# Kernel tuning notes

Measured on AMD Instinct MI355X. Metric: run time of the kernel, lower is better.

The kernel has to match this reference:

```python
import jax, jax.numpy as jnp
import numpy as np

B, S, D, H = 2, 1024, 1024, 8
HD = D // H            # head_dim = 128
NBUCKETS = 64          # bucket_size (number of hash buckets)
NEG = -1e30


def setup_inputs() -> dict:
    key = jax.random.key(0)
    ks = jax.random.split(key, 10)
    scale = D ** -0.5
    return {
        "x": jax.random.normal(ks[0], (B, S, D), dtype=jnp.float32),
        "Wq": jax.random.normal(ks[1], (D, D), dtype=jnp.float32) * scale,
        "bq": jnp.zeros((D,), dtype=jnp.float32),
        "Wk": jax.random.normal(ks[2], (D, D), dtype=jnp.float32) * scale,
        "bk": jnp.zeros((D,), dtype=jnp.float32),
        "Wv": jax.random.normal(ks[3], (D, D), dtype=jnp.float32) * scale,
        "bv": jnp.zeros((D,), dtype=jnp.float32),
        "Wo": jax.random.normal(ks[4], (D, D), dtype=jnp.float32) * scale,
        "bo": jnp.zeros((D,), dtype=jnp.float32),
        "hash_proj": jax.random.normal(ks[5], (H, HD, NBUCKETS), dtype=jnp.float32),
    }


def reference(x, Wq, bq, Wk, bk, Wv, bv, Wo, bo, hash_proj):
    b, s, d = x.shape
    n = b * s  # buckets gather (batch, token) pairs jointly -> flatten batch into tokens

    def split_heads(y):  # [B,S,D] -> [H, B*S, HD]
        return y.reshape(b, s, H, HD).transpose(2, 0, 1, 3).reshape(H, n, HD)

    q = split_heads(x @ Wq + bq)
    k = split_heads(x @ Wk + bk)
    v = split_heads(x @ Wv + bv)

    # learned LSH routing: argmax over hash projections per head
    hash_scores = jnp.einsum('hnd,hdf->hnf', q, hash_proj)
    buckets = jnp.argmax(hash_scores, axis=-1)  # [H, N] int

    # per-bucket attention == masked dense attention with same-bucket mask
    dots = jnp.einsum('hnd,hmd->hnm', q, k) / (HD ** 0.5)  # [H,N,N]
    same = buckets[:, :, None] == buckets[:, None, :]
    attn = jax.nn.softmax(jnp.where(same, dots, NEG), axis=-1)
    o = jnp.einsum('hnm,hmd->hnd', attn, v)  # [H,N,HD]

    out = o.reshape(H, b, s, HD).transpose(1, 2, 0, 3).reshape(b, s, d)
    return out @ Wo + bo
```

## Files before the change

### kernel.cpp

```cpp
#include <hip/hip_runtime.h>
#include <stdint.h>

typedef __attribute__((ext_vector_type(8))) short short8;
typedef __attribute__((ext_vector_type(4))) short short4v;
typedef __attribute__((ext_vector_type(4))) float float4v;
typedef unsigned short u16;

#define N_TOK 2048
#define D_MODEL 1024
#define N_HEAD 8
#define HDIM 128
#define N_BUCKET 64
#define WL_CAP 2048
#define ATTN_BLOCKS 384

__device__ __forceinline__ u16 f2bf(float f) {
  uint32_t u = __float_as_uint(f);
  uint32_t r = u + 0x7fffu + ((u >> 16) & 1u);
  return (u16)(r >> 16);
}
__device__ __forceinline__ float bf2f(u16 h) {
  return __uint_as_float(((uint32_t)h) << 16);
}

__device__ __forceinline__ void async_load16(const void* g, void* l) {
  __builtin_amdgcn_global_load_lds(
      (const __attribute__((address_space(1))) void*)g,
      (__attribute__((address_space(3))) void*)l, 16, 0, 0);
}

__device__ __forceinline__ int xcd_swz(int bid, int nwg) {
  return (bid & 7) * (nwg >> 3) + (bid >> 3);
}

__global__ __launch_bounds__(256) void split_cast_kernel(
    const float* __restrict__ in, u16* __restrict__ hi, u16* __restrict__ lo,
    int n) {
  int i = blockIdx.x * 256 + threadIdx.x;
  if (i >= n) return;
  float v = in[i];
  u16 h = f2bf(v);
  hi[i] = h;
  if (lo) lo[i] = f2bf(v - bf2f(h));
}

__global__ __launch_bounds__(256) void transpose_all_kernel(
    const float* __restrict__ Wq, const float* __restrict__ Wk,
    const float* __restrict__ Wv, const float* __restrict__ Wo,
    u16* __restrict__ wqt_hi, u16* __restrict__ wqt_lo,
    u16* __restrict__ kvt, u16* __restrict__ wot) {
  __shared__ float tile[32][33];
  const int z = blockIdx.z;
  const float* in = (z == 0) ? Wq : (z == 1) ? Wk : (z == 2) ? Wv : Wo;
  u16* hi = (z == 0) ? wqt_hi
            : (z == 1) ? kvt
            : (z == 2) ? (kvt + (size_t)1024 * 1024) : wot;
  u16* lo = (z == 0) ? wqt_lo : nullptr;
  const int C = 1024, R = 1024;
  int c0 = blockIdx.x * 32, r0 = blockIdx.y * 32;
  int tx = threadIdx.x & 31, ty = threadIdx.x >> 5;
#pragma unroll
  for (int i = 0; i < 4; i++) {
    int rl = ty + i * 8;
    tile[rl][tx] = in[(size_t)(r0 + rl) * C + c0 + tx];
  }
  __syncthreads();
#pragma unroll
  for (int i = 0; i < 4; i++) {
    int cl = ty + i * 8;
    float v = tile[tx][cl];
    size_t oidx = (size_t)(c0 + cl) * R + r0 + tx;
    u16 h = f2bf(v);
    hi[oidx] = h;
    if (lo) lo[oidx] = f2bf(v - bf2f(h));
  }
}

template <int BM>
__device__ __forceinline__ void stage_tiles2(const u16* A, const u16* Bt,
                                             u16* As, u16* Bs, int bm, int bn,
                                             int K, int ko, int wave, int lane) {
  const int arow = lane >> 2;
  const int acolb = (lane & 3) * 16;
  constexpr int ACH = BM / 16;
  constexpr int PC = (ACH + 8) / 4;
#pragma unroll
  for (int cc = 0; cc < PC; cc++) {
    int idx = wave * PC + cc;
    if (idx < ACH) {
      int row = idx * 16 + arow;
      const char* g = (const char*)A + ((size_t)(bm + row) * K + ko) * 2 + acolb;
      async_load16(g, (char*)As + idx * 1024);
    } else {
      int row = (idx - ACH) * 16 + arow;
      const char* g = (const char*)Bt + ((size_t)(bn + row) * K + ko) * 2 + acolb;
      async_load16(g, (char*)Bs + (idx - ACH) * 1024);
    }
  }
}

template <int BM>
__global__ __launch_bounds__(256) void gemm_bf16_kernel(
    const u16* __restrict__ A, const u16* __restrict__ Bt,
    float* __restrict__ C, const float* __restrict__ bias,
    const float* __restrict__ bias2, u16* __restrict__ kbf,
    u16* __restrict__ vbf, int N, int K, int flags) {
  constexpr int MI = BM / 32;
  __shared__ __align__(16) u16 As[2][BM * 32];
  __shared__ __align__(16) u16 Bs[2][128 * 32];
  const int tid = threadIdx.x;
  const int wave = tid >> 6, lane = tid & 63;
  const int lhi = lane >> 4, llo = lane & 15;
  const int nbn = N >> 7;
  const int bid = xcd_swz(blockIdx.x, gridDim.x);
  const int bm = (bid / nbn) * BM;
  const int bn = (bid % nbn) << 7;
  const int wm = (BM == 128) ? (wave >> 1) * 64 : (wave & 1) * 32;
  const int wn = (BM == 128) ? (wave & 1) * 64 : (wave >> 1) * 64;

  float4v acc[MI][4];
#pragma unroll
  for (int mi = 0; mi < MI; mi++)
#pragma unroll
    for (int ni = 0; ni < 4; ni++)
#pragma unroll
      for (int r = 0; r < 4; r++) acc[mi][ni][r] = 0.f;

  stage_tiles2<BM>(A, Bt, As[0], Bs[0], bm, bn, K, 0, wave, lane);
  __syncthreads();
  const int nk = K >> 5;
  for (int t = 0; t < nk; t++) {
    const int cur = t & 1;
    if (t + 1 < nk)
      stage_tiles2<BM>(A, Bt, As[cur ^ 1], Bs[cur ^ 1], bm, bn, K,
                       (t + 1) << 5, wave, lane);
    short8 af[MI], bfr[4];
#pragma unroll
    for (int i = 0; i < MI; i++)
      af[i] = *(const short8*)&As[cur][(wm + i * 16 + llo) * 32 + lhi * 8];
#pragma unroll
    for (int i = 0; i < 4; i++)
      bfr[i] = *(const short8*)&Bs[cur][(wn + i * 16 + llo) * 32 + lhi * 8];
#pragma unroll
    for (int mi = 0; mi < MI; mi++)
#pragma unroll
      for (int ni = 0; ni < 4; ni++)
        acc[mi][ni] = __builtin_amdgcn_mfma_f32_16x16x32_bf16(af[mi], bfr[ni],
                                                              acc[mi][ni], 0, 0, 0);
    __syncthreads();
  }

#pragma unroll
  for (int mi = 0; mi < MI; mi++)
#pragma unroll
    for (int ni = 0; ni < 4; ni++) {
      int row0 = bm + wm + mi * 16 + lhi * 4;
      int col = bn + wn + ni * 16 + llo;
      if (flags & 8) {
        u16* dst = (col < 1024) ? kbf : vbf;
        int c = col & 1023;
        float bb = (col < 1024) ? bias[c] : bias2[c];
#pragma unroll
        for (int r = 0; r < 4; r++)
          dst[(size_t)(row0 + r) * 1024 + c] = f2bf(acc[mi][ni][r] + bb);
      } else {
        float bb = (flags & 2) ? bias[col] : 0.f;
        float* cp = C + (size_t)row0 * N + col;
#pragma unroll
        for (int r = 0; r < 4; r++) cp[(size_t)r * N] = acc[mi][ni][r] + bb;
      }
    }
}

__global__ __launch_bounds__(256) void gemm3_bf16_kernel(
    const u16* __restrict__ A0, const u16* __restrict__ A1,
    const u16* __restrict__ B0, const u16* __restrict__ B1,
    float* __restrict__ C, const float* __restrict__ bias,
    u16* __restrict__ bf_out, int N, int K) {
  constexpr int MI = 2;
  __shared__ __align__(16) u16 S3[2][12288];
  const int tid = threadIdx.x;
  const int wave = tid >> 6, lane = tid & 63;
  const int lhi = lane >> 4, llo = lane & 15;
  const int nbn = N >> 7;
  const int bid = xcd_swz(blockIdx.x, gridDim.x);
  const int bm = (bid / nbn) * 64;
  const int bn = (bid % nbn) << 7;
  const int wm = (wave & 1) * 32;
  const int wn = (wave >> 1) * 64;
  const int arow = lane >> 2;
  const int acolb = (lane & 3) * 16;

  float4v acc[MI][4];
#pragma unroll
  for (int mi = 0; mi < MI; mi++)
#pragma unroll
    for (int ni = 0; ni < 4; ni++)
#pragma unroll
      for (int r = 0; r < 4; r++) acc[mi][ni][r] = 0.f;

  auto stage = [&](int b, int ko) {
    char* base = (char*)&S3[b][0];
#pragma unroll
    for (int cc = 0; cc < 6; cc++) {
      int idx = wave * 6 + cc;
      const u16* src;
      int row;
      char* dst;
      if (idx < 4) {
        src = A0; row = bm + idx * 16 + arow; dst = base + idx * 1024;
      } else if (idx < 8) {
        src = A1; row = bm + (idx - 4) * 16 + arow; dst = base + 4096 + (idx - 4) * 1024;
      } else if (idx < 16) {
        src = B0; row = bn + (idx - 8) * 16 + arow; dst = base + 8192 + (idx - 8) * 1024;
      } else {
        src = B1; row = bn + (idx - 16) * 16 + arow; dst = base + 16384 + (idx - 16) * 1024;
      }
      async_load16((const char*)src + ((size_t)row * K + ko) * 2 + acolb, dst);
    }
  };

  stage(0, 0);
  __syncthreads();
  const int nk = K >> 5;
  for (int t = 0; t < nk; t++) {
    const int cur = t & 1;
    if (t + 1 < nk) stage(cur ^ 1, (t + 1) << 5);
    const u16* Sc = &S3[cur][0];
    short8 afh[MI], afl[MI], bfh[4], bfl[4];
#pragma unroll
    for (int i = 0; i < MI; i++) {
      afh[i] = *(const short8*)&Sc[(wm + i * 16 + llo) * 32 + lhi * 8];
      afl[i] = *(const short8*)&Sc[2048 + (wm + i * 16 + llo) * 32 + lhi * 8];
    }
#pragma unroll
    for (int i = 0; i < 4; i++) {
      bfh[i] = *(const short8*)&Sc[4096 + (wn + i * 16 + llo) * 32 + lhi * 8];
      bfl[i] = *(const short8*)&Sc[8192 + (wn + i * 16 + llo) * 32 + lhi * 8];
    }
#pragma unroll
    for (int mi = 0; mi < MI; mi++)
#pragma unroll
      for (int ni = 0; ni < 4; ni++)
        acc[mi][ni] = __builtin_amdgcn_mfma_f32_16x16x32_bf16(afh[mi], bfh[ni],
                                                              acc[mi][ni], 0, 0, 0);
#pragma unroll
    for (int mi = 0; mi < MI; mi++)
#pragma unroll
      for (int ni = 0; ni < 4; ni++)
        acc[mi][ni] = __builtin_amdgcn_mfma_f32_16x16x32_bf16(afh[mi], bfl[ni],
                                                              acc[mi][ni], 0, 0, 0);
#pragma unroll
    for (int mi = 0; mi < MI; mi++)
#pragma unroll
      for (int ni = 0; ni < 4; ni++)
        acc[mi][ni] = __builtin_amdgcn_mfma_f32_16x16x32_bf16(afl[mi], bfh[ni],
                                                              acc[mi][ni], 0, 0, 0);
    __syncthreads();
  }

#pragma unroll
  for (int mi = 0; mi < MI; mi++)
#pragma unroll
    for (int ni = 0; ni < 4; ni++) {
      int row0 = bm + wm + mi * 16 + lhi * 4;
      int col = bn + wn + ni * 16 + llo;
      float bb = bias[col];
#pragma unroll
      for (int r = 0; r < 4; r++) {
        float v = acc[mi][ni][r] + bb;
        C[(size_t)(row0 + r) * N + col] = v;
        bf_out[(size_t)(row0 + r) * N + col] = f2bf(v);
      }
    }
}

__global__ __launch_bounds__(256) void hash_argmax_kernel(
    const float* __restrict__ Qf, const float* __restrict__ proj,
    int* __restrict__ bucket) {
  __shared__ float sQ[64 * 128];
  __shared__ float sP[128 * 64];
  const int tid = threadIdx.x;
  const int h = blockIdx.y;
  const int n0 = blockIdx.x * 64;
#pragma unroll
  for (int p = 0; p < 8; p++) {
    int e = p * 1024 + tid * 4;
    int tok = e >> 7, d0 = e & 127;
    float4v v = *(const float4v*)&Qf[(size_t)(n0 + tok) * D_MODEL + h * HDIM + d0];
    int blk = (d0 >> 2) ^ ((tok >> 2) & 7);
    *(float4v*)&sQ[tok * 128 + blk * 4] = v;
  }
#pragma unroll
  for (int p = 0; p < 8; p++) {
    int e = p * 1024 + tid * 4;
    float4v v = *(const float4v*)&proj[(size_t)h * (HDIM * N_BUCKET) + e];
    *(float4v*)&sP[e] = v;
  }
  __syncthreads();

  const int tgrp = tid & 15, fgrp = tid >> 4;
  const int t0 = tgrp * 4, f0 = fgrp * 4;
  float accs[4][4];
#pragma unroll
  for (int i = 0; i < 4; i++)
#pragma unroll
    for (int f = 0; f < 4; f++) accs[i][f] = 0.f;

  for (int d0 = 0; d0 < 128; d0 += 4) {
    int blk = (d0 >> 2) ^ (tgrp & 7);
    float4v qv[4], pv[4];
#pragma unroll
    for (int i = 0; i < 4; i++)
      qv[i] = *(const float4v*)&sQ[(t0 + i) * 128 + blk * 4];
#pragma unroll
    for (int j = 0; j < 4; j++)
      pv[j] = *(const float4v*)&sP[(d0 + j) * 64 + f0];
#pragma unroll
    for (int i = 0; i < 4; i++)
#pragma unroll
      for (int f = 0; f < 4; f++)
        accs[i][f] += qv[i][0] * pv[0][f] + qv[i][1] * pv[1][f] +
                      qv[i][2] * pv[2][f] + qv[i][3] * pv[3][f];
  }

  __syncthreads();
  float* vals = sQ;
  int* idxs = (int*)(sQ + 64 * 17);
#pragma unroll
  for (int i = 0; i < 4; i++) {
    float bv = accs[i][0];
    int bi = f0;
#pragma unroll
    for (int f = 1; f < 4; f++)
      if (accs[i][f] > bv) { bv = accs[i][f]; bi = f0 + f; }
    vals[(t0 + i) * 17 + fgrp] = bv;
    idxs[(t0 + i) * 17 + fgrp] = bi;
  }
  __syncthreads();
  if (tid < 64) {
    float bv = vals[tid * 17];
    int bi = idxs[tid * 17];
#pragma unroll
    for (int g = 1; g < 16; g++) {
      float v = vals[tid * 17 + g];
      int id = idxs[tid * 17 + g];
      if (v > bv || (v == bv && id < bi)) { bv = v; bi = id; }
    }
    bucket[h * N_TOK + n0 + tid] = bi;
  }
}

__global__ __launch_bounds__(64) void bucket_count_kernel(
    const int* __restrict__ bucket, int* __restrict__ counts) {
  int hb = blockIdx.x;
  int h = hb >> 6, b = hb & 63;
  int lane = threadIdx.x;
  int cnt = 0;
  for (int t = 0; t < N_TOK; t += 64) {
    bool match = bucket[h * N_TOK + t + lane] == b;
    unsigned long long mask = __ballot(match);
    cnt += __popcll(mask);
  }
  if (lane == 0) counts[hb] = cnt;
}

__global__ __launch_bounds__(512) void build_wl_kernel(
    const int* __restrict__ counts, int* __restrict__ offsets,
    int* __restrict__ wl, int* __restrict__ wl_count) {
  __shared__ int sc[512];
  int tid = threadIdx.x;
  int cnt = counts[tid];
  sc[tid] = cnt;
  __syncthreads();
  for (int o = 1; o < 512; o <<= 1) {
    int v = (tid >= o) ? sc[tid - o] : 0;
    __syncthreads();
    sc[tid] += v;
    __syncthreads();
  }
  offsets[tid] = sc[tid] - cnt;
  __syncthreads();
  int nq = (cnt + 15) >> 4;
  sc[tid] = nq;
  __syncthreads();
  for (int o = 1; o < 512; o <<= 1) {
    int v = (tid >= o) ? sc[tid - o] : 0;
    __syncthreads();
    sc[tid] += v;
    __syncthreads();
  }
  int base = sc[tid] - nq;
  int h = tid >> 6, b = tid & 63;
  for (int i = 0; i < nq; i++) wl[base + i] = (h << 13) | (b << 7) | i;
  if (tid == 511) wl_count[0] = sc[511];
}

__global__ __launch_bounds__(64) void bucket_fill_kernel(
    const int* __restrict__ bucket, const int* __restrict__ offsets,
    int* __restrict__ perm) {
  int hb = blockIdx.x;
  int h = hb >> 6, b = hb & 63;
  int lane = threadIdx.x;
  int base = offsets[hb];
  for (int t = 0; t < N_TOK; t += 64) {
    int tok = t + lane;
    bool match = bucket[h * N_TOK + tok] == b;
    unsigned long long mask = __ballot(match);
    if (match) {
      int pos = base + __popcll(mask & ((1ull << lane) - 1ull));
      perm[pos] = tok;
    }
    base += __popcll(mask);
  }
}

__global__ __launch_bounds__(256) void gather_vt_kernel(
    const u16* __restrict__ vbb, const int* __restrict__ perm,
    u16* __restrict__ Vts) {
  __shared__ u16 lds[64][72];
  int bid = blockIdx.x;
  int h = bid >> 6;
  int ptile = (bid & 63) >> 1;
  int d0 = (bid & 1) * 64;
  int pos0 = ptile * 64;
  int t = threadIdx.x;
#pragma unroll
  for (int i = 0; i < 2; i++) {
    int unit = t + 256 * i;
    int p = unit >> 3, seg = unit & 7;
    int tok = perm[h * N_TOK + pos0 + p];
    short8 v = *(const short8*)&vbb[(size_t)tok * D_MODEL + h * HDIM + d0 + seg * 8];
    *(short8*)&lds[p][seg * 8] = v;
  }
  __syncthreads();
#pragma unroll
  for (int i = 0; i < 8; i++) {
    int unit = t + 256 * i;
    int drow = unit >> 5, pp = unit & 31;
    uint32_t val = (uint32_t)lds[2 * pp][drow] |
                   ((uint32_t)lds[2 * pp + 1][drow] << 16);
    uint32_t* dst = (uint32_t*)&Vts[(size_t)(h * HDIM + d0 + drow) * N_TOK + pos0];
    dst[pp] = val;
  }
}

__global__ __launch_bounds__(256) void attn_bucket_kernel(
    const u16* __restrict__ qbb, const u16* __restrict__ kbb,
    const u16* __restrict__ Vts, const int* __restrict__ perm,
    const int* __restrict__ offsets, const int* __restrict__ counts,
    const int* __restrict__ wl, const int* __restrict__ wl_count,
    u16* __restrict__ ob) {
  const int wave = threadIdx.x >> 6, lane = threadIdx.x & 63;
  const int lhi = lane >> 4, llo = lane & 15;
  const int wslot = blockIdx.x * 4 + wave;
  const int NW = ATTN_BLOCKS * 4;
  const int cnt = wl_count[0];
  __shared__ __align__(16) u16 P_lds[4][16][64];
  const float scale = 0.08838834764831845f;

  for (int e = wslot; e < cnt; e += NW) {
    int ent = wl[e];
    int h = ent >> 13, qt = ent & 127;
    int hb = (h << 6) | ((ent >> 7) & 63);
    int off = offsets[hb];
    int bs = counts[hb];
    int offh = off - h * N_TOK;
    int qbase = qt * 16;

    int qr = qbase + llo;
    int tokq = perm[off + min(qr, bs - 1)];
    const u16* qrow = &qbb[(size_t)tokq * D_MODEL + h * HDIM];
    short8 qf[4];
#pragma unroll
    for (int kf = 0; kf < 4; kf++)
      qf[kf] = *(const short8*)&qrow[kf * 32 + lhi * 8];

    float m[4], l[4];
#pragma unroll
    for (int r = 0; r < 4; r++) { m[r] = -INFINITY; l[r] = 0.f; }
    float4v accO[8];
#pragma unroll
    for (int d = 0; d < 8; d++)
#pragma unroll
      for (int r = 0; r < 4; r++) accO[d][r] = 0.f;

    for (int c0 = 0; c0 < bs; c0 += 64) {
      float4v sc[4];
#pragma unroll
      for (int nf = 0; nf < 4; nf++)
#pragma unroll
        for (int r = 0; r < 4; r++) sc[nf][r] = 0.f;
#pragma unroll
      for (int nf = 0; nf < 4; nf++) {
        int kcol = c0 + nf * 16 + llo;
        int tokk = perm[off + min(kcol, bs - 1)];
        const u16* krow = &kbb[(size_t)tokk * D_MODEL + h * HDIM];
#pragma unroll
        for (int kf = 0; kf < 4; kf++) {
          short8 kfr = *(const short8*)&krow[kf * 32 + lhi * 8];
          sc[nf] = __builtin_amdgcn_mfma_f32_16x16x32_bf16(qf[kf], kfr, sc[nf], 0, 0, 0);
        }
      }

      float tmax[4];
#pragma unroll
      for (int r = 0; r < 4; r++) tmax[r] = -INFINITY;
#pragma unroll
      for (int nf = 0; nf < 4; nf++) {
        bool valid = (c0 + nf * 16 + llo) < bs;
#pragma unroll
        for (int r = 0; r < 4; r++) {
          float v = valid ? sc[nf][r] * scale : -1e30f;
          sc[nf][r] = v;
          tmax[r] = fmaxf(tmax[r], v);
        }
      }
#pragma unroll
      for (int r = 0; r < 4; r++)
#pragma unroll
        for (int o = 1; o < 16; o <<= 1)
          tmax[r] = fmaxf(tmax[r], __shfl_xor(tmax[r], o));

      float resc[4], psum[4];
#pragma unroll
      for (int r = 0; r < 4; r++) {
        float mn = fmaxf(m[r], tmax[r]);
        resc[r] = __expf(m[r] - mn);
        m[r] = mn;
        psum[r] = 0.f;
      }
#pragma unroll
      for (int nf = 0; nf < 4; nf++)
#pragma unroll
        for (int r = 0; r < 4; r++) {
          float p = __expf(sc[nf][r] - m[r]);
          psum[r] += p;
          P_lds[wave][lhi * 4 + r][nf * 16 + llo] = f2bf(p);
        }
#pragma unroll
      for (int r = 0; r < 4; r++) {
#pragma unroll
        for (int o = 1; o < 16; o <<= 1) psum[r] += __shfl_xor(psum[r], o);
        l[r] = l[r] * resc[r] + psum[r];
      }
#pragma unroll
      for (int d = 0; d < 8; d++)
#pragma unroll
        for (int r = 0; r < 4; r++) accO[d][r] *= resc[r];

      asm volatile("s_waitcnt lgkmcnt(0)" ::: "memory");
      short8 pf[2];
#pragma unroll
      for (int k2 = 0; k2 < 2; k2++)
        pf[k2] = *(const short8*)&P_lds[wave][llo][k2 * 32 + lhi * 8];
#pragma unroll
      for (int d = 0; d < 8; d++)
#pragma unroll
        for (int k2 = 0; k2 < 2; k2++) {
          short8 vfr = *(const short8*)&Vts[(size_t)(h * HDIM + d * 16 + llo) * N_TOK +
                                            offh + c0 + k2 * 32 + lhi * 8];
          accO[d] = __builtin_amdgcn_mfma_f32_16x16x32_bf16(pf[k2], vfr, accO[d], 0, 0, 0);
        }
      asm volatile("" ::: "memory");
    }

#pragma unroll
    for (int r = 0; r < 4; r++) {
      int rl = qbase + lhi * 4 + r;
      if (rl < bs) {
        int tok = perm[off + rl];
        float inv = 1.f / l[r];
#pragma unroll
        for (int d = 0; d < 8; d++)
          ob[(size_t)tok * D_MODEL + h * HDIM + d * 16 + llo] = f2bf(accO[d][r] * inv);
      }
    }
  }
}

extern "C" void kernel_launch(void* const* d_in, const int* in_sizes, int n_in,
                              void* d_out, int out_size, void* d_ws, size_t ws_size,
                              hipStream_t stream) {
  const float* x  = (const float*)d_in[0];
  const float* Wq = (const float*)d_in[1];
  const float* bq = (const float*)d_in[2];
  const float* Wk = (const float*)d_in[3];
  const float* bk = (const float*)d_in[4];
  const float* Wv = (const float*)d_in[5];
  const float* bv = (const float*)d_in[6];
  const float* Wo = (const float*)d_in[7];
  const float* bo = (const float*)d_in[8];
  const float* hp = (const float*)d_in[9];
  float* out = (float*)d_out;

  char* ws = (char*)d_ws;
  size_t off = 0;
  auto alloc = [&](size_t b) {
    char* p = ws + off;
    off += (b + 255) & ~(size_t)255;
    return p;
  };

  const int N = N_TOK, D = D_MODEL;
  u16* xhi    = (u16*)alloc((size_t)N * D * 2);
  u16* xlo    = (u16*)alloc((size_t)N * D * 2);
  u16* wqt_hi = (u16*)alloc((size_t)D * D * 2);
  u16* wqt_lo = (u16*)alloc((size_t)D * D * 2);
  u16* kvt    = (u16*)alloc((size_t)2 * D * D * 2);
  u16* wot    = (u16*)alloc((size_t)D * D * 2);
  float* Qf   = (float*)alloc((size_t)N * D * 4);
  u16* qbb    = (u16*)alloc((size_t)N * D * 2);
  u16* kbb    = (u16*)alloc((size_t)N * D * 2);
  u16* vbb    = (u16*)alloc((size_t)N * D * 2);
  u16* Vts    = (u16*)alloc((size_t)N_HEAD * HDIM * N * 2 + 256);
  int* bucket = (int*)alloc((size_t)N_HEAD * N * 4);
  int* counts = (int*)alloc(512 * 4);
  int* offs   = (int*)alloc(512 * 4);
  int* perm   = (int*)alloc((size_t)N_HEAD * N * 4);
  int* wl     = (int*)alloc(WL_CAP * 4);
  int* wlcnt  = (int*)alloc(256);
  u16* ob     = (u16*)alloc((size_t)N * D * 2);

  const int nelem = N * D;

  split_cast_kernel<<<(nelem + 255) / 256, 256, 0, stream>>>(x, xhi, xlo, nelem);
  transpose_all_kernel<<<dim3(32, 32, 4), 256, 0, stream>>>(
      Wq, Wk, Wv, Wo, wqt_hi, wqt_lo, kvt, wot);

  gemm3_bf16_kernel<<<(N / 64) * (D / 128), 256, 0, stream>>>(
      xhi, xlo, wqt_hi, wqt_lo, Qf, bq, qbb, D, D);
  gemm_bf16_kernel<64><<<(N / 64) * (2 * D / 128), 256, 0, stream>>>(
      xhi, kvt, nullptr, bk, bv, kbb, vbb, 2 * D, D, 2 | 8);

  hash_argmax_kernel<<<dim3(N / 64, N_HEAD), 256, 0, stream>>>(Qf, hp, bucket);
  bucket_count_kernel<<<512, 64, 0, stream>>>(bucket, counts);
  build_wl_kernel<<<1, 512, 0, stream>>>(counts, offs, wl, wlcnt);
  bucket_fill_kernel<<<512, 64, 0, stream>>>(bucket, offs, perm);
  gather_vt_kernel<<<512, 256, 0, stream>>>(vbb, perm, Vts);

  attn_bucket_kernel<<<ATTN_BLOCKS, 256, 0, stream>>>(
      qbb, kbb, Vts, perm, offs, counts, wl, wlcnt, ob);

  gemm_bf16_kernel<64><<<(N / 64) * (D / 128), 256, 0, stream>>>(
      ob, wot, out, bo, nullptr, nullptr, nullptr, D, D, 2);

  (void)in_sizes; (void)n_in; (void)out_size; (void)ws_size;
}
```

Baseline: 131.7 us.

## Fuse input prep kernels and merge bucket count/scan/fill into one sort kernel

Merges the x split-cast and the weight transposes into a single launch that uses an extra grid z-slice, with vectorized casting of x. Replaces the three bucketing kernels (count, worklist build, fill) with one 512-thread block sort_kernel. It uses ballot-based match masks to count and scatter each head's tokens in shared memory. This removes several kernel launches and intermediate global round-trips. In exchange, the sort runs on a single workgroup and loops serially over 2048 tokens per wave.

```diff
diff --git a/kernel.cpp b/kernel.cpp
--- a/kernel.cpp
+++ b/kernel.cpp
@@ -33,24 +33,35 @@
   return (bid & 7) * (nwg >> 3) + (bid >> 3);
 }
 
-__global__ __launch_bounds__(256) void split_cast_kernel(
-    const float* __restrict__ in, u16* __restrict__ hi, u16* __restrict__ lo,
-    int n) {
-  int i = blockIdx.x * 256 + threadIdx.x;
-  if (i >= n) return;
-  float v = in[i];
-  u16 h = f2bf(v);
-  hi[i] = h;
-  if (lo) lo[i] = f2bf(v - bf2f(h));
-}
-
-__global__ __launch_bounds__(256) void transpose_all_kernel(
-    const float* __restrict__ Wq, const float* __restrict__ Wk,
-    const float* __restrict__ Wv, const float* __restrict__ Wo,
-    u16* __restrict__ wqt_hi, u16* __restrict__ wqt_lo,
-    u16* __restrict__ kvt, u16* __restrict__ wot) {
+__global__ __launch_bounds__(256) void prep_kernel(
+    const float* __restrict__ x, const float* __restrict__ Wq,
+    const float* __restrict__ Wk, const float* __restrict__ Wv,
+    const float* __restrict__ Wo, u16* __restrict__ xhi, u16* __restrict__ xlo,
+    u16* __restrict__ wqt_hi, u16* __restrict__ wqt_lo, u16* __restrict__ kvt,
+    u16* __restrict__ wot) {
+  const int z = blockIdx.z;
+  if (z == 4) {
+    int base = (blockIdx.y * 32 + blockIdx.x) * 2048 + threadIdx.x * 8;
+    float4v a = *(const float4v*)&x[base];
+    float4v b = *(const float4v*)&x[base + 4];
+    short8 hi, lo;
+#pragma unroll
+    for (int j = 0; j < 4; j++) {
+      u16 h = f2bf(a[j]);
+      hi[j] = (short)h;
+      lo[j] = (short)f2bf(a[j] - bf2f(h));
+    }
+#pragma unroll
+    for (int j = 0; j < 4; j++) {
+      u16 h = f2bf(b[j]);
+      hi[4 + j] = (short)h;
+      lo[4 + j] = (short)f2bf(b[j] - bf2f(h));
+    }
+    *(short8*)&xhi[base] = hi;
+    *(short8*)&xlo[base] = lo;
+    return;
+  }
   __shared__ float tile[32][33];
-  const int z = blockIdx.z;
   const float* in = (z == 0) ? Wq : (z == 1) ? Wk : (z == 2) ? Wv : Wo;
   u16* hi = (z == 0) ? wqt_hi
             : (z == 1) ? kvt
@@ -351,27 +362,35 @@
   }
 }
 
-__global__ __launch_bounds__(64) void bucket_count_kernel(
-    const int* __restrict__ bucket, int* __restrict__ counts) {
-  int hb = blockIdx.x;
-  int h = hb >> 6, b = hb & 63;
-  int lane = threadIdx.x;
-  int cnt = 0;
+__device__ __forceinline__ unsigned long long match_mask(int b) {
+  unsigned long long mask = ~0ull;
+#pragma unroll
+  for (int bit = 0; bit < 6; bit++) {
+    unsigned long long vt = __ballot((b >> bit) & 1);
+    mask &= ((b >> bit) & 1) ? vt : ~vt;
+  }
+  return mask;
+}
+
+__global__ __launch_bounds__(512) void sort_kernel(
+    const int* __restrict__ bucket, int* __restrict__ counts_g,
+    int* __restrict__ offsets_g, int* __restrict__ perm,
+    int* __restrict__ wl, int* __restrict__ wl_count) {
+  __shared__ int cnt[512];
+  __shared__ int sc[512];
+  __shared__ int run[512];
+  const int tid = threadIdx.x;
+  const int w = tid >> 6, lane = tid & 63;
+  cnt[tid] = 0;
+  __syncthreads();
   for (int t = 0; t < N_TOK; t += 64) {
-    bool match = bucket[h * N_TOK + t + lane] == b;
-    unsigned long long mask = __ballot(match);
-    cnt += __popcll(mask);
-  }
-  if (lane == 0) counts[hb] = cnt;
-}
-
-__global__ __launch_bounds__(512) void build_wl_kernel(
-    const int* __restrict__ counts, int* __restrict__ offsets,
-    int* __restrict__ wl, int* __restrict__ wl_count) {
-  __shared__ int sc[512];
-  int tid = threadIdx.x;
-  int cnt = counts[tid];
-  sc[tid] = cnt;
+    int b = bucket[w * N_TOK + t + lane];
+    unsigned long long mask = match_mask(b);
+    if (lane == __ffsll(mask) - 1) cnt[w * 64 + b] += __popcll(mask);
+  }
+  __syncthreads();
+  int c = cnt[tid];
+  sc[tid] = c;
   __syncthreads();
   for (int o = 1; o < 512; o <<= 1) {
     int v = (tid >= o) ? sc[tid - o] : 0;
@@ -379,9 +398,12 @@
     sc[tid] += v;
     __syncthreads();
   }
-  offsets[tid] = sc[tid] - cnt;
-  __syncthreads();
-  int nq = (cnt + 15) >> 4;
+  int off0 = sc[tid] - c;
+  offsets_g[tid] = off0;
+  counts_g[tid] = c;
+  run[tid] = off0;
+  __syncthreads();
+  int nq = (c + 15) >> 4;
   sc[tid] = nq;
   __syncthreads();
   for (int o = 1; o < 512; o <<= 1) {
@@ -391,27 +413,18 @@
     __syncthreads();
   }
   int base = sc[tid] - nq;
-  int h = tid >> 6, b = tid & 63;
-  for (int i = 0; i < nq; i++) wl[base + i] = (h << 13) | (b << 7) | i;
+  int hh = tid >> 6, bb = tid & 63;
+  for (int i = 0; i < nq; i++) wl[base + i] = (hh << 13) | (bb << 7) | i;
   if (tid == 511) wl_count[0] = sc[511];
-}
-
-__global__ __launch_bounds__(64) void bucket_fill_kernel(
-    const int* __restrict__ bucket, const int* __restrict__ offsets,
-    int* __restrict__ perm) {
-  int hb = blockIdx.x;
-  int h = hb >> 6, b = hb & 63;
-  int lane = threadIdx.x;
-  int base = offsets[hb];
+  __syncthreads();
   for (int t = 0; t < N_TOK; t += 64) {
     int tok = t + lane;
-    bool match = bucket[h * N_TOK + tok] == b;
-    unsigned long long mask = __ballot(match);
-    if (match) {
-      int pos = base + __popcll(mask & ((1ull << lane) - 1ull));
-      perm[pos] = tok;
-    }
-    base += __popcll(mask);
+    int b = bucket[w * N_TOK + tok];
+    unsigned long long mask = match_mask(b);
+    int lower = __popcll(mask & ((1ull << lane) - 1ull));
+    int pos = run[w * 64 + b] + lower;
+    perm[pos] = tok;
+    if (lane == __ffsll(mask) - 1) run[w * 64 + b] += __popcll(mask);
   }
 }
 
@@ -486,11 +499,11 @@
       for (int r = 0; r < 4; r++) accO[d][r] = 0.f;
 
     for (int c0 = 0; c0 < bs; c0 += 64) {
-      float4v sc[4];
+      float4v scv[4];
 #pragma unroll
       for (int nf = 0; nf < 4; nf++)
 #pragma unroll
-        for (int r = 0; r < 4; r++) sc[nf][r] = 0.f;
+        for (int r = 0; r < 4; r++) scv[nf][r] = 0.f;
 #pragma unroll
       for (int nf = 0; nf < 4; nf++) {
         int kcol = c0 + nf * 16 + llo;
@@ -499,7 +512,7 @@
 #pragma unroll
         for (int kf = 0; kf < 4; kf++) {
           short8 kfr = *(const short8*)&krow[kf * 32 + lhi * 8];
-          sc[nf] = __builtin_amdgcn_mfma_f32_16x16x32_bf16(qf[kf], kfr, sc[nf], 0, 0, 0);
+          scv[nf] = __builtin_amdgcn_mfma_f32_16x16x32_bf16(qf[kf], kfr, scv[nf], 0, 0, 0);
         }
       }
 
@@ -511,8 +524,8 @@
         bool valid = (c0 + nf * 16 + llo) < bs;
 #pragma unroll
         for (int r = 0; r < 4; r++) {
-          float v = valid ? sc[nf][r] * scale : -1e30f;
-          sc[nf][r] = v;
+          float v = valid ? scv[nf][r] * scale : -1e30f;
+          scv[nf][r] = v;
           tmax[r] = fmaxf(tmax[r], v);
         }
       }
@@ -534,7 +547,7 @@
       for (int nf = 0; nf < 4; nf++)
 #pragma unroll
         for (int r = 0; r < 4; r++) {
-          float p = __expf(sc[nf][r] - m[r]);
+          float p = __expf(scv[nf][r] - m[r]);
           psum[r] += p;
           P_lds[wave][lhi * 4 + r][nf * 16 + llo] = f2bf(p);
         }
@@ -622,11 +635,8 @@
   int* wlcnt  = (int*)alloc(256);
   u16* ob     = (u16*)alloc((size_t)N * D * 2);
 
-  const int nelem = N * D;
-
-  split_cast_kernel<<<(nelem + 255) / 256, 256, 0, stream>>>(x, xhi, xlo, nelem);
-  transpose_all_kernel<<<dim3(32, 32, 4), 256, 0, stream>>>(
-      Wq, Wk, Wv, Wo, wqt_hi, wqt_lo, kvt, wot);
+  prep_kernel<<<dim3(32, 32, 5), 256, 0, stream>>>(
+      x, Wq, Wk, Wv, Wo, xhi, xlo, wqt_hi, wqt_lo, kvt, wot);
 
   gemm3_bf16_kernel<<<(N / 64) * (D / 128), 256, 0, stream>>>(
       xhi, xlo, wqt_hi, wqt_lo, Qf, bq, qbb, D, D);
@@ -634,9 +644,7 @@
       xhi, kvt, nullptr, bk, bv, kbb, vbb, 2 * D, D, 2 | 8);
 
   hash_argmax_kernel<<<dim3(N / 64, N_HEAD), 256, 0, stream>>>(Qf, hp, bucket);
-  bucket_count_kernel<<<512, 64, 0, stream>>>(bucket, counts);
-  build_wl_kernel<<<1, 512, 0, stream>>>(counts, offs, wl, wlcnt);
-  bucket_fill_kernel<<<512, 64, 0, stream>>>(bucket, offs, perm);
+  sort_kernel<<<1, 512, 0, stream>>>(bucket, counts, offs, perm, wl, wlcnt);
   gather_vt_kernel<<<512, 256, 0, stream>>>(vbb, perm, Vts);
 
   attn_bucket_kernel<<<ATTN_BLOCKS, 256, 0, stream>>>(
```

Result: slower. 146.8 us (+11.5%).

## Fuse hash argmax into Q projection epilogue and merge prep kernels

Applied to the files above, without the earlier changes.

The fp32 Q tile is kept in LDS after the Q GEMM, and each block computes the per-head hash projection and argmax directly in its epilogue. This removes the fp32 Qf buffer write/read and the separate hash kernel launch. The x split-cast is also folded into the weight transpose launch as an extra grid slice with vectorized loads. The trade-off is that the epilogue hash loop reads proj from global memory per thread with a serial 128-step loop, which may be slower than the old tiled LDS version.

```diff
diff --git a/kernel.cpp b/kernel.cpp
--- a/kernel.cpp
+++ b/kernel.cpp
@@ -33,24 +33,35 @@
   return (bid & 7) * (nwg >> 3) + (bid >> 3);
 }
 
-__global__ __launch_bounds__(256) void split_cast_kernel(
-    const float* __restrict__ in, u16* __restrict__ hi, u16* __restrict__ lo,
-    int n) {
-  int i = blockIdx.x * 256 + threadIdx.x;
-  if (i >= n) return;
-  float v = in[i];
-  u16 h = f2bf(v);
-  hi[i] = h;
-  if (lo) lo[i] = f2bf(v - bf2f(h));
-}
-
-__global__ __launch_bounds__(256) void transpose_all_kernel(
-    const float* __restrict__ Wq, const float* __restrict__ Wk,
-    const float* __restrict__ Wv, const float* __restrict__ Wo,
-    u16* __restrict__ wqt_hi, u16* __restrict__ wqt_lo,
-    u16* __restrict__ kvt, u16* __restrict__ wot) {
+__global__ __launch_bounds__(256) void prep_kernel(
+    const float* __restrict__ x, const float* __restrict__ Wq,
+    const float* __restrict__ Wk, const float* __restrict__ Wv,
+    const float* __restrict__ Wo, u16* __restrict__ xhi, u16* __restrict__ xlo,
+    u16* __restrict__ wqt_hi, u16* __restrict__ wqt_lo, u16* __restrict__ kvt,
+    u16* __restrict__ wot) {
+  const int z = blockIdx.z;
+  if (z == 4) {
+    int base = (blockIdx.y * 32 + blockIdx.x) * 2048 + threadIdx.x * 8;
+    float4v a = *(const float4v*)&x[base];
+    float4v b = *(const float4v*)&x[base + 4];
+    short8 hi, lo;
+#pragma unroll
+    for (int j = 0; j < 4; j++) {
+      u16 h = f2bf(a[j]);
+      hi[j] = (short)h;
+      lo[j] = (short)f2bf(a[j] - bf2f(h));
+    }
+#pragma unroll
+    for (int j = 0; j < 4; j++) {
+      u16 h = f2bf(b[j]);
+      hi[4 + j] = (short)h;
+      lo[4 + j] = (short)f2bf(b[j] - bf2f(h));
+    }
+    *(short8*)&xhi[base] = hi;
+    *(short8*)&xlo[base] = lo;
+    return;
+  }
   __shared__ float tile[32][33];
-  const int z = blockIdx.z;
   const float* in = (z == 0) ? Wq : (z == 1) ? Wk : (z == 2) ? Wv : Wo;
   u16* hi = (z == 0) ? wqt_hi
             : (z == 1) ? kvt
@@ -175,8 +186,8 @@
 __global__ __launch_bounds__(256) void gemm3_bf16_kernel(
     const u16* __restrict__ A0, const u16* __restrict__ A1,
     const u16* __restrict__ B0, const u16* __restrict__ B1,
-    float* __restrict__ C, const float* __restrict__ bias,
-    u16* __restrict__ bf_out, int N, int K) {
+    const float* __restrict__ proj, const float* __restrict__ bias,
+    u16* __restrict__ bf_out, int* __restrict__ bucket, int N, int K) {
   constexpr int MI = 2;
   __shared__ __align__(16) u16 S3[2][12288];
   const int tid = threadIdx.x;
@@ -259,95 +270,56 @@
     __syncthreads();
   }
 
+  float* sQf = (float*)&S3[0][0];
 #pragma unroll
   for (int mi = 0; mi < MI; mi++)
 #pragma unroll
     for (int ni = 0; ni < 4; ni++) {
-      int row0 = bm + wm + mi * 16 + lhi * 4;
-      int col = bn + wn + ni * 16 + llo;
-      float bb = bias[col];
+      int rl0 = wm + mi * 16 + lhi * 4;
+      int col = wn + ni * 16 + llo;
+      float bb = bias[bn + col];
 #pragma unroll
       for (int r = 0; r < 4; r++) {
         float v = acc[mi][ni][r] + bb;
-        C[(size_t)(row0 + r) * N + col] = v;
-        bf_out[(size_t)(row0 + r) * N + col] = f2bf(v);
-      }
-    }
-}
-
-__global__ __launch_bounds__(256) void hash_argmax_kernel(
-    const float* __restrict__ Qf, const float* __restrict__ proj,
-    int* __restrict__ bucket) {
-  __shared__ float sQ[64 * 128];
-  __shared__ float sP[128 * 64];
-  const int tid = threadIdx.x;
-  const int h = blockIdx.y;
-  const int n0 = blockIdx.x * 64;
-#pragma unroll
-  for (int p = 0; p < 8; p++) {
-    int e = p * 1024 + tid * 4;
-    int tok = e >> 7, d0 = e & 127;
-    float4v v = *(const float4v*)&Qf[(size_t)(n0 + tok) * D_MODEL + h * HDIM + d0];
-    int blk = (d0 >> 2) ^ ((tok >> 2) & 7);
-    *(float4v*)&sQ[tok * 128 + blk * 4] = v;
-  }
-#pragma unroll
-  for (int p = 0; p < 8; p++) {
-    int e = p * 1024 + tid * 4;
-    float4v v = *(const float4v*)&proj[(size_t)h * (HDIM * N_BUCKET) + e];
-    *(float4v*)&sP[e] = v;
-  }
-  __syncthreads();
-
-  const int tgrp = tid & 15, fgrp = tid >> 4;
-  const int t0 = tgrp * 4, f0 = fgrp * 4;
-  float accs[4][4];
-#pragma unroll
-  for (int i = 0; i < 4; i++)
-#pragma unroll
-    for (int f = 0; f < 4; f++) accs[i][f] = 0.f;
-
-  for (int d0 = 0; d0 < 128; d0 += 4) {
-    int blk = (d0 >> 2) ^ (tgrp & 7);
-    float4v qv[4], pv[4];
-#pragma unroll
-    for (int i = 0; i < 4; i++)
-      qv[i] = *(const float4v*)&sQ[(t0 + i) * 128 + blk * 4];
-#pragma unroll
-    for (int j = 0; j < 4; j++)
-      pv[j] = *(const float4v*)&sP[(d0 + j) * 64 + f0];
-#pragma unroll
-    for (int i = 0; i < 4; i++)
-#pragma unroll
-      for (int f = 0; f < 4; f++)
-        accs[i][f] += qv[i][0] * pv[0][f] + qv[i][1] * pv[1][f] +
-                      qv[i][2] * pv[2][f] + qv[i][3] * pv[3][f];
-  }
-
-  __syncthreads();
-  float* vals = sQ;
-  int* idxs = (int*)(sQ + 64 * 17);
-#pragma unroll
-  for (int i = 0; i < 4; i++) {
-    float bv = accs[i][0];
-    int bi = f0;
-#pragma unroll
-    for (int f = 1; f < 4; f++)
-      if (accs[i][f] > bv) { bv = accs[i][f]; bi = f0 + f; }
-    vals[(t0 + i) * 17 + fgrp] = bv;
-    idxs[(t0 + i) * 17 + fgrp] = bi;
-  }
-  __syncthreads();
-  if (tid < 64) {
-    float bv = vals[tid * 17];
-    int bi = idxs[tid * 17];
-#pragma unroll
-    for (int g = 1; g < 16; g++) {
-      float v = vals[tid * 17 + g];
-      int id = idxs[tid * 17 + g];
-      if (v > bv || (v == bv && id < bi)) { bv = v; bi = id; }
-    }
-    bucket[h * N_TOK + n0 + tid] = bi;
+        bf_out[(size_t)(bm + rl0 + r) * N + bn + col] = f2bf(v);
+        sQf[(rl0 + r) * 129 + col] = v;
+      }
+    }
+  __syncthreads();
+
+  {
+    const int tok = tid >> 2, grp = tid & 3;
+    const int h = bn >> 7;
+    const float* pp = proj + (size_t)h * (HDIM * N_BUCKET) + grp * 16;
+    float a16[16];
+#pragma unroll
+    for (int j = 0; j < 16; j++) a16[j] = 0.f;
+    for (int d = 0; d < 128; d++) {
+      float qd = sQf[tok * 129 + d];
+      float4v p0 = *(const float4v*)&pp[d * 64 + 0];
+      float4v p1 = *(const float4v*)&pp[d * 64 + 4];
+      float4v p2 = *(const float4v*)&pp[d * 64 + 8];
+      float4v p3 = *(const float4v*)&pp[d * 64 + 12];
+#pragma unroll
+      for (int j = 0; j < 4; j++) {
+        a16[j] += qd * p0[j];
+        a16[4 + j] += qd * p1[j];
+        a16[8 + j] += qd * p2[j];
+        a16[12 + j] += qd * p3[j];
+      }
+    }
+    float best = a16[0];
+    int bi = grp * 16;
+#pragma unroll
+    for (int j = 1; j < 16; j++)
+      if (a16[j] > best) { best = a16[j]; bi = grp * 16 + j; }
+#pragma unroll
+    for (int o = 1; o < 4; o <<= 1) {
+      float ov = __shfl_xor(best, o);
+      int oi = __shfl_xor(bi, o);
+      if (ov > best || (ov == best && oi < bi)) { best = ov; bi = oi; }
+    }
+    if (grp == 0) bucket[h * N_TOK + bm + tok] = bi;
   }
 }
 
@@ -486,11 +458,11 @@
       for (int r = 0; r < 4; r++) accO[d][r] = 0.f;
 
     for (int c0 = 0; c0 < bs; c0 += 64) {
-      float4v sc[4];
+      float4v scv[4];
 #pragma unroll
       for (int nf = 0; nf < 4; nf++)
 #pragma unroll
-        for (int r = 0; r < 4; r++) sc[nf][r] = 0.f;
+        for (int r = 0; r < 4; r++) scv[nf][r] = 0.f;
 #pragma unroll
       for (int nf = 0; nf < 4; nf++) {
         int kcol = c0 + nf * 16 + llo;
@@ -499,7 +471,7 @@
 #pragma unroll
         for (int kf = 0; kf < 4; kf++) {
           short8 kfr = *(const short8*)&krow[kf * 32 + lhi * 8];
-          sc[nf] = __builtin_amdgcn_mfma_f32_16x16x32_bf16(qf[kf], kfr, sc[nf], 0, 0, 0);
+          scv[nf] = __builtin_amdgcn_mfma_f32_16x16x32_bf16(qf[kf], kfr, scv[nf], 0, 0, 0);
         }
       }
 
@@ -511,8 +483,8 @@
         bool valid = (c0 + nf * 16 + llo) < bs;
 #pragma unroll
         for (int r = 0; r < 4; r++) {
-          float v = valid ? sc[nf][r] * scale : -1e30f;
-          sc[nf][r] = v;
+          float v = valid ? scv[nf][r] * scale : -1e30f;
+          scv[nf][r] = v;
           tmax[r] = fmaxf(tmax[r], v);
         }
       }
@@ -534,7 +506,7 @@
       for (int nf = 0; nf < 4; nf++)
 #pragma unroll
         for (int r = 0; r < 4; r++) {
-          float p = __expf(sc[nf][r] - m[r]);
+          float p = __expf(scv[nf][r] - m[r]);
           psum[r] += p;
           P_lds[wave][lhi * 4 + r][nf * 16 + llo] = f2bf(p);
         }
@@ -609,7 +581,6 @@
   u16* wqt_lo = (u16*)alloc((size_t)D * D * 2);
   u16* kvt    = (u16*)alloc((size_t)2 * D * D * 2);
   u16* wot    = (u16*)alloc((size_t)D * D * 2);
-  float* Qf   = (float*)alloc((size_t)N * D * 4);
   u16* qbb    = (u16*)alloc((size_t)N * D * 2);
   u16* kbb    = (u16*)alloc((size_t)N * D * 2);
   u16* vbb    = (u16*)alloc((size_t)N * D * 2);
@@ -622,18 +593,14 @@
   int* wlcnt  = (int*)alloc(256);
   u16* ob     = (u16*)alloc((size_t)N * D * 2);
 
-  const int nelem = N * D;
-
-  split_cast_kernel<<<(nelem + 255) / 256, 256, 0, stream>>>(x, xhi, xlo, nelem);
-  transpose_all_kernel<<<dim3(32, 32, 4), 256, 0, stream>>>(
-      Wq, Wk, Wv, Wo, wqt_hi, wqt_lo, kvt, wot);
+  prep_kernel<<<dim3(32, 32, 5), 256, 0, stream>>>(
+      x, Wq, Wk, Wv, Wo, xhi, xlo, wqt_hi, wqt_lo, kvt, wot);
 
   gemm3_bf16_kernel<<<(N / 64) * (D / 128), 256, 0, stream>>>(
-      xhi, xlo, wqt_hi, wqt_lo, Qf, bq, qbb, D, D);
+      xhi, xlo, wqt_hi, wqt_lo, hp, bq, qbb, bucket, D, D);
   gemm_bf16_kernel<64><<<(N / 64) * (2 * D / 128), 256, 0, stream>>>(
       xhi, kvt, nullptr, bk, bv, kbb, vbb, 2 * D, D, 2 | 8);
 
-  hash_argmax_kernel<<<dim3(N / 64, N_HEAD), 256, 0, stream>>>(Qf, hp, bucket);
   bucket_count_kernel<<<512, 64, 0, stream>>>(bucket, counts);
   build_wl_kernel<<<1, 512, 0, stream>>>(counts, offs, wl, wlcnt);
   bucket_fill_kernel<<<512, 64, 0, stream>>>(bucket, offs, perm);
```

Result: slower. 147.0 us (+11.7%).
